# Performance work log

Hardware: AMD Instinct MI355X
Metric: run time of the kernel (lower is better)

Reference implementation:

```python
import jax, jax.numpy as jnp
import numpy as np

NUM_HEADS = 16
D_MODEL = 1024
BATCH = 4
SEQ = 1024


def setup_inputs() -> dict:
    key = jax.random.key(0)
    k_x, k_m, k_wqkv, k_bqkv, k_wo, k_bo = jax.random.split(key, 6)
    d = D_MODEL
    scale = 1.0 / np.sqrt(d)
    return {
        "x": jax.random.normal(k_x, (BATCH, SEQ, d), dtype=jnp.float32),
        "mask": jax.random.randint(k_m, (BATCH, SEQ, SEQ), 0, 2, dtype=jnp.int32),
        "Wqkv": jax.random.normal(k_wqkv, (d, 3 * d), dtype=jnp.float32) * scale,
        "bqkv": jax.random.normal(k_bqkv, (3 * d,), dtype=jnp.float32) * 0.02,
        "Wo": jax.random.normal(k_wo, (d, d), dtype=jnp.float32) * scale,
        "bo": jax.random.normal(k_bo, (d,), dtype=jnp.float32) * 0.02,
    }


def reference(x, mask, Wqkv, bqkv, Wo, bo):
    B, S, D = x.shape
    H = NUM_HEADS
    hd = D // H
    # fused QKV projection: [B,S,3D] -> [B,S,H,3*hd] -> [B,H,S,3*hd]
    qkv = (x @ Wqkv + bqkv).reshape(B, S, H, 3 * hd).transpose(0, 2, 1, 3)
    q, k, v = jnp.split(qkv, 3, axis=-1)  # each [B,H,S,hd]
    # scores [B,H,S,S], scaled by sqrt(head_dim)
    scores = jnp.einsum("bhqd,bhkd->bhqk", q, k) / jnp.sqrt(jnp.float32(hd))
    scores = jnp.where(mask[:, None, :, :] == 0, jnp.float32(-1e20), scores)
    attn = jax.nn.softmax(scores, axis=-1)
    vals = jnp.einsum("bhqk,bhkd->bhqd", attn, v)  # [B,H,S,hd]
    vals = vals.transpose(0, 2, 1, 3).reshape(B, S, D)
    return vals @ Wo + bo
```

## Files before the change

kernel.cpp:

```cpp
#include <hip/hip_runtime.h>
#include <cstddef>
#include <cstdint>

#define BATCH 4
#define SEQ   1024
#define DM    1024
#define NH    16
#define HD    64
#define D3    3072
#define LOG2E 1.44269504088896340736f
#define QSCALE (0.125f * LOG2E)

typedef _Float16 f16x8 __attribute__((ext_vector_type(8)));
typedef _Float16 f16x4 __attribute__((ext_vector_type(4)));
typedef __fp16   h16x2 __attribute__((ext_vector_type(2)));
typedef float    f32x4 __attribute__((ext_vector_type(4)));

#define MFMA16(a, b, c) __builtin_amdgcn_mfma_f32_16x16x32_f16((a), (b), (c), 0, 0, 0)
#define GLD_LDS16(gp, lp) \
  __builtin_amdgcn_global_load_lds((const __attribute__((address_space(1))) unsigned int*)(gp), \
                                   (__attribute__((address_space(3))) unsigned int*)(lp), 16, 0, 0)
#if __has_builtin(__builtin_amdgcn_exp2f)
#define EXP2(x) __builtin_amdgcn_exp2f(x)
#else
#define EXP2(x) exp2f(x)
#endif

__global__ __launch_bounds__(256) void cast_f16(const float* __restrict__ in,
                                                _Float16* __restrict__ out, int n8) {
  int i = blockIdx.x * 256 + threadIdx.x;
  if (i >= n8) return;
  float4 a = ((const float4*)in)[i * 2];
  float4 b = ((const float4*)in)[i * 2 + 1];
  f16x8 o;
  o[0] = (_Float16)a.x; o[1] = (_Float16)a.y; o[2] = (_Float16)a.z; o[3] = (_Float16)a.w;
  o[4] = (_Float16)b.x; o[5] = (_Float16)b.y; o[6] = (_Float16)b.z; o[7] = (_Float16)b.w;
  ((f16x8*)out)[i] = o;
}

__global__ __launch_bounds__(256) void transpose_cast(const float* __restrict__ W,
                                                      _Float16* __restrict__ WT,
                                                      int K, int N) {
  __shared__ _Float16 T[64 * 72];
  const int tid = threadIdx.x;
  const int r0 = blockIdx.y * 64, c0 = blockIdx.x * 64;
#pragma unroll
  for (int it = 0; it < 4; ++it) {
    const int row = it * 16 + (tid >> 4);
    const int col4 = (tid & 15) * 4;
    float4 wv = *(const float4*)(W + (size_t)(r0 + row) * N + c0 + col4);
    T[(col4 + 0) * 72 + row] = (_Float16)wv.x;
    T[(col4 + 1) * 72 + row] = (_Float16)wv.y;
    T[(col4 + 2) * 72 + row] = (_Float16)wv.z;
    T[(col4 + 3) * 72 + row] = (_Float16)wv.w;
  }
  __syncthreads();
#pragma unroll
  for (int it = 0; it < 2; ++it) {
    const int g = it * 256 + tid;
    const int col = g >> 3, seg = g & 7;
    *(f16x8*)(WT + (size_t)(c0 + col) * K + r0 + seg * 8) = *(const f16x8*)(T + col * 72 + seg * 8);
  }
}

__global__ __launch_bounds__(256) void pack_mask(const int* __restrict__ mask,
                                                 unsigned long long* __restrict__ mb) {
  const size_t i = (size_t)blockIdx.x * 256 + threadIdx.x;
  const int m = mask[i];
  unsigned long long bits = __ballot(m != 0);
  if ((threadIdx.x & 63) == 0) mb[i >> 6] = bits;
}

template <typename OutT, bool QKV, int TN>
__global__ __launch_bounds__(256) void gemm_bt(const _Float16* __restrict__ A,
                                               const _Float16* __restrict__ BT,
                                               const float* __restrict__ bias,
                                               OutT* __restrict__ C,
                                               _Float16* __restrict__ vTp,
                                               int M, int N, int K) {
  constexpr int NT = TN / 32;
  __shared__ _Float16 As[128 * 32];
  __shared__ _Float16 Bs[TN * 32];
  const int tid = threadIdx.x;
  const int l15 = tid & 15;
  const int quad = (tid & 63) >> 4;
  const int w = tid >> 6;
  const int wm = w >> 1, wn = w & 1;
  const int rowbase = blockIdx.y * 128;
  const int colbase = blockIdx.x * TN;

  f32x4 acc[4][NT];
#pragma unroll
  for (int mt = 0; mt < 4; ++mt)
#pragma unroll
    for (int nt = 0; nt < NT; ++nt) acc[mt][nt] = (f32x4){0.f, 0.f, 0.f, 0.f};

  const int g0 = tid, g1 = 256 + tid;
  const _Float16* Ag0 = A + (size_t)(rowbase + (g0 >> 2)) * K + (g0 & 3) * 8;
  const _Float16* Ag1 = A + (size_t)(rowbase + (g1 >> 2)) * K + (g1 & 3) * 8;
  const _Float16* Bg0 = BT + (size_t)(colbase + (g0 >> 2)) * K + (g0 & 3) * 8;
  const _Float16* Bg1 = BT + (size_t)(colbase + ((g1 >> 2) & (TN - 1))) * K + (g1 & 3) * 8;

  for (int k0 = 0; k0 < K; k0 += 32) {
    __syncthreads();
    GLD_LDS16(Ag0 + k0, As + g0 * 8);
    GLD_LDS16(Ag1 + k0, As + g1 * 8);
    GLD_LDS16(Bg0 + k0, Bs + g0 * 8);
    if constexpr (TN == 128) GLD_LDS16(Bg1 + k0, Bs + g1 * 8);
    __syncthreads();
    f16x8 a[4], b[NT];
#pragma unroll
    for (int mt = 0; mt < 4; ++mt)
      a[mt] = *(const f16x8*)(As + (wm * 64 + mt * 16 + l15) * 32 + quad * 8);
#pragma unroll
    for (int nt = 0; nt < NT; ++nt)
      b[nt] = *(const f16x8*)(Bs + (wn * (TN / 2) + nt * 16 + l15) * 32 + quad * 8);
#pragma unroll
    for (int mt = 0; mt < 4; ++mt)
#pragma unroll
      for (int nt = 0; nt < NT; ++nt)
        acc[mt][nt] = MFMA16(a[mt], b[nt], acc[mt][nt]);
  }

  float bv[NT];
#pragma unroll
  for (int nt = 0; nt < NT; ++nt) bv[nt] = bias[colbase + wn * (TN / 2) + nt * 16 + l15];
#pragma unroll
  for (int mt = 0; mt < 4; ++mt)
#pragma unroll
    for (int nt = 0; nt < NT; ++nt) {
      const int col = colbase + wn * (TN / 2) + nt * 16 + l15;
      if (QKV) {
        const int reg3 = (col >> 6) % 3;
        if (reg3 == 2) {
          const int hh = col / 192;
          const int d = col - hh * 192 - 128;
          const int row0 = rowbase + wm * 64 + mt * 16 + quad * 4;
          const int bb = row0 >> 10, s0 = row0 & 1023;
          f16x4 pk;
#pragma unroll
          for (int r = 0; r < 4; ++r) pk[r] = (_Float16)(acc[mt][nt][r] + bv[nt]);
          *(f16x4*)(vTp + ((size_t)((bb * NH + hh) * HD + d)) * SEQ + s0) = pk;
        } else {
          const float sc = (reg3 == 0) ? QSCALE : 1.f;
#pragma unroll
          for (int r = 0; r < 4; ++r) {
            const int row = rowbase + wm * 64 + mt * 16 + quad * 4 + r;
            C[(size_t)row * N + col] = (OutT)((acc[mt][nt][r] + bv[nt]) * sc);
          }
        }
      } else {
#pragma unroll
        for (int r = 0; r < 4; ++r) {
          const int row = rowbase + wm * 64 + mt * 16 + quad * 4 + r;
          C[(size_t)row * N + col] = (OutT)(acc[mt][nt][r] + bv[nt]);
        }
      }
    }
}

__global__ __launch_bounds__(256) void attn(const _Float16* __restrict__ qkv,
                                            const _Float16* __restrict__ vT,
                                            const unsigned long long* __restrict__ mb,
                                            _Float16* __restrict__ vals) {
  __shared__ _Float16 Ks[64 * 72];
  __shared__ _Float16 Vt[64 * 72];
  __shared__ _Float16 Ps[4][32 * 72];
  __shared__ __align__(8) _Float16 LUT[16][4];
  const int tid = threadIdx.x;
  const int l15 = tid & 15, quad = (tid & 63) >> 4, w = tid >> 6;
  const int b = blockIdx.y >> 4, h = blockIdx.y & 15;
  const int q0 = blockIdx.x << 7;

  if (tid < 16) {
    LUT[tid][0] = (tid & 1) ? (_Float16)1.f : (_Float16)0.f;
    LUT[tid][1] = (tid & 2) ? (_Float16)1.f : (_Float16)0.f;
    LUT[tid][2] = (tid & 4) ? (_Float16)1.f : (_Float16)0.f;
    LUT[tid][3] = (tid & 8) ? (_Float16)1.f : (_Float16)0.f;
  }

  const _Float16* qb = qkv + (size_t)b * SEQ * D3 + h * 192;
  f16x8 qf[2][2];
#pragma unroll
  for (int qn = 0; qn < 2; ++qn)
#pragma unroll
    for (int hf = 0; hf < 2; ++hf)
      qf[qn][hf] = *(const f16x8*)(qb + (size_t)(q0 + w * 32 + qn * 16 + l15) * D3 +
                                   hf * 32 + quad * 8);

  const _Float16* kg = qb + 64;
  const _Float16* vg = vT + (size_t)((b * NH + h) * HD) * SEQ;
  const int sr = tid >> 3, sseg = tid & 7;
  const int vd = tid >> 2, vs = tid & 3;
  const size_t mb0 = (size_t)(b * SEQ + q0 + w * 32 + l15) * 16;
  const size_t mb1 = (size_t)(b * SEQ + q0 + w * 32 + 16 + l15) * 16;

  f16x8 k0r = *(const f16x8*)(kg + (size_t)sr * D3 + sseg * 8);
  f16x8 k1r = *(const f16x8*)(kg + (size_t)(sr + 32) * D3 + sseg * 8);
  f16x8 v0r = *(const f16x8*)(vg + (size_t)vd * SEQ + vs * 8);
  f16x8 v1r = *(const f16x8*)(vg + (size_t)vd * SEQ + 32 + vs * 8);
  unsigned long long mr0 = mb[mb0], mr1 = mb[mb1];

  f32x4 lacc[2];
  f32x4 o_[2][4];
#pragma unroll
  for (int qn = 0; qn < 2; ++qn) {
    lacc[qn] = (f32x4){0.f, 0.f, 0.f, 0.f};
#pragma unroll
    for (int dt = 0; dt < 4; ++dt) o_[qn][dt] = (f32x4){0.f, 0.f, 0.f, 0.f};
  }
  f16x8 ones;
#pragma unroll
  for (int i = 0; i < 8; ++i) ones[i] = (_Float16)1.f;

  for (int kt = 0; kt < 16; ++kt) {
    if (kt) __syncthreads();
    *(f16x8*)(Ks + sr * 72 + sseg * 8) = k0r;
    *(f16x8*)(Ks + (sr + 32) * 72 + sseg * 8) = k1r;
    *(f16x8*)(Vt + vd * 72 + vs * 8) = v0r;
    *(f16x8*)(Vt + vd * 72 + 32 + vs * 8) = v1r;
    __syncthreads();
    const unsigned long long mc[2] = {mr0, mr1};
    if (kt < 15) {
      const int kn = (kt + 1) << 6;
      k0r = *(const f16x8*)(kg + (size_t)(kn + sr) * D3 + sseg * 8);
      k1r = *(const f16x8*)(kg + (size_t)(kn + sr + 32) * D3 + sseg * 8);
      v0r = *(const f16x8*)(vg + (size_t)vd * SEQ + kn + vs * 8);
      v1r = *(const f16x8*)(vg + (size_t)vd * SEQ + kn + 32 + vs * 8);
      mr0 = mb[mb0 + kt + 1];
      mr1 = mb[mb1 + kt + 1];
    }
    f32x4 st[4][2];
#pragma unroll
    for (int mt = 0; mt < 4; ++mt)
#pragma unroll
      for (int qn = 0; qn < 2; ++qn) st[mt][qn] = (f32x4){0.f, 0.f, 0.f, 0.f};
#pragma unroll
    for (int mt = 0; mt < 4; ++mt) {
      f16x8 ka0 = *(const f16x8*)(Ks + (mt * 16 + l15) * 72 + quad * 8);
      f16x8 ka1 = *(const f16x8*)(Ks + (mt * 16 + l15) * 72 + 32 + quad * 8);
#pragma unroll
      for (int qn = 0; qn < 2; ++qn) {
        st[mt][qn] = MFMA16(ka0, qf[qn][0], st[mt][qn]);
        st[mt][qn] = MFMA16(ka1, qf[qn][1], st[mt][qn]);
      }
    }
#pragma unroll
    for (int qn = 0; qn < 2; ++qn)
#pragma unroll
      for (int mt = 0; mt < 4; ++mt) {
        float e0 = EXP2(fminf(st[mt][qn][0], 15.f));
        float e1 = EXP2(fminf(st[mt][qn][1], 15.f));
        float e2 = EXP2(fminf(st[mt][qn][2], 15.f));
        float e3 = EXP2(fminf(st[mt][qn][3], 15.f));
        h16x2 lo = __builtin_amdgcn_cvt_pkrtz(e0, e1);
        h16x2 hi = __builtin_amdgcn_cvt_pkrtz(e2, e3);
        f16x4 pk;
        pk[0] = (_Float16)lo[0]; pk[1] = (_Float16)lo[1];
        pk[2] = (_Float16)hi[0]; pk[3] = (_Float16)hi[1];
        const unsigned nib = (unsigned)(mc[qn] >> (mt * 16 + quad * 4)) & 15u;
        pk *= *(const f16x4*)LUT[nib];
        *(f16x4*)(&Ps[w][(qn * 16 + l15) * 72 + mt * 16 + quad * 4]) = pk;
      }
    f16x8 pa[2][2];
#pragma unroll
    for (int qn = 0; qn < 2; ++qn) {
      pa[qn][0] = *(const f16x8*)(&Ps[w][(qn * 16 + l15) * 72 + quad * 8]);
      pa[qn][1] = *(const f16x8*)(&Ps[w][(qn * 16 + l15) * 72 + 32 + quad * 8]);
      lacc[qn] = MFMA16(pa[qn][0], ones, lacc[qn]);
      lacc[qn] = MFMA16(pa[qn][1], ones, lacc[qn]);
    }
#pragma unroll
    for (int dt = 0; dt < 4; ++dt) {
      f16x8 vb0 = *(const f16x8*)(Vt + (dt * 16 + l15) * 72 + quad * 8);
      f16x8 vb1 = *(const f16x8*)(Vt + (dt * 16 + l15) * 72 + 32 + quad * 8);
#pragma unroll
      for (int qn = 0; qn < 2; ++qn) {
        o_[qn][dt] = MFMA16(pa[qn][0], vb0, o_[qn][dt]);
        o_[qn][dt] = MFMA16(pa[qn][1], vb1, o_[qn][dt]);
      }
    }
  }
#pragma unroll
  for (int qn = 0; qn < 2; ++qn) {
    f32x4 inv;
#pragma unroll
    for (int r = 0; r < 4; ++r) inv[r] = 1.f / lacc[qn][r];
#pragma unroll
    for (int dt = 0; dt < 4; ++dt)
#pragma unroll
      for (int r = 0; r < 4; ++r)
        vals[(size_t)(b * SEQ + q0 + w * 32 + qn * 16 + quad * 4 + r) * DM +
             h * HD + dt * 16 + l15] = (_Float16)(o_[qn][dt][r] * inv[r]);
  }
}

extern "C" void kernel_launch(void* const* d_in, const int* in_sizes, int n_in,
                              void* d_out, int out_size, void* d_ws, size_t ws_size,
                              hipStream_t stream) {
  const float* x    = (const float*)d_in[0];
  const int*   mask = (const int*)  d_in[1];
  const float* Wqkv = (const float*)d_in[2];
  const float* bqkv = (const float*)d_in[3];
  const float* Wo   = (const float*)d_in[4];
  const float* bo   = (const float*)d_in[5];
  float* out = (float*)d_out;

  char* ws = (char*)d_ws;
  _Float16* qkv16  = (_Float16*)ws;                    ws += (size_t)BATCH*SEQ*D3*2;
  _Float16* vT16   = (_Float16*)ws;                    ws += (size_t)BATCH*DM*SEQ*2;
  _Float16* x16    = (_Float16*)ws;                    ws += (size_t)BATCH*SEQ*DM*2;
  _Float16* WqkvT  = (_Float16*)ws;                    ws += (size_t)DM*D3*2;
  _Float16* WoT    = (_Float16*)ws;                    ws += (size_t)DM*DM*2;
  _Float16* vals16 = (_Float16*)ws;                    ws += (size_t)BATCH*SEQ*DM*2;
  unsigned long long* mbits = (unsigned long long*)ws;

  cast_f16<<<(BATCH*SEQ*DM/8 + 255)/256, 256, 0, stream>>>(x, x16, BATCH*SEQ*DM/8);
  transpose_cast<<<dim3(D3/64, DM/64), 256, 0, stream>>>(Wqkv, WqkvT, DM, D3);
  transpose_cast<<<dim3(DM/64, DM/64), 256, 0, stream>>>(Wo, WoT, DM, DM);
  pack_mask<<<(BATCH*SEQ*SEQ)/256, 256, 0, stream>>>(mask, mbits);

  gemm_bt<_Float16, true, 128><<<dim3(D3/128, BATCH*SEQ/128), 256, 0, stream>>>(
      x16, WqkvT, bqkv, qkv16, vT16, BATCH*SEQ, D3, DM);
  attn<<<dim3(SEQ/128, BATCH*NH), 256, 0, stream>>>(qkv16, vT16, mbits, vals16);
  gemm_bt<float, false, 64><<<dim3(DM/64, (BATCH*SEQ)/128), 256, 0, stream>>>(
      vals16, WoT, bo, out, nullptr, BATCH*SEQ, DM, DM);
}
```

Baseline: 203.1 us.

## Merge prep kernels, deepen GEMM K-tile with swizzled LDS, remap attention grid

Fuses the x cast and mask packing into one launch, and the two weight transposes into another, cutting the number of kernel launches. The GEMM now stages 64-wide K tiles with an XOR-swizzled LDS layout, which halves barrier count and avoids bank conflicts, at the cost of more LDS per block. The attention grid becomes 1D with a block-index remap that groups heads, intended to improve L2 locality for the mask and K/V.

```diff
diff --git a/kernel.cpp b/kernel.cpp
--- a/kernel.cpp
+++ b/kernel.cpp
@@ -26,24 +26,40 @@
 #define EXP2(x) exp2f(x)
 #endif
 
-__global__ __launch_bounds__(256) void cast_f16(const float* __restrict__ in,
-                                                _Float16* __restrict__ out, int n8) {
-  int i = blockIdx.x * 256 + threadIdx.x;
-  if (i >= n8) return;
-  float4 a = ((const float4*)in)[i * 2];
-  float4 b = ((const float4*)in)[i * 2 + 1];
-  f16x8 o;
-  o[0] = (_Float16)a.x; o[1] = (_Float16)a.y; o[2] = (_Float16)a.z; o[3] = (_Float16)a.w;
-  o[4] = (_Float16)b.x; o[5] = (_Float16)b.y; o[6] = (_Float16)b.z; o[7] = (_Float16)b.w;
-  ((f16x8*)out)[i] = o;
-}
-
-__global__ __launch_bounds__(256) void transpose_cast(const float* __restrict__ W,
-                                                      _Float16* __restrict__ WT,
-                                                      int K, int N) {
+__global__ __launch_bounds__(256) void prep(const float* __restrict__ x,
+                                            _Float16* __restrict__ x16,
+                                            const int* __restrict__ mask,
+                                            unsigned long long* __restrict__ mb) {
+  const int tid = threadIdx.x;
+  if (blockIdx.x < 2048) {
+    const int i = blockIdx.x * 256 + tid;
+    float4 a = ((const float4*)x)[i * 2];
+    float4 b = ((const float4*)x)[i * 2 + 1];
+    f16x8 o;
+    o[0] = (_Float16)a.x; o[1] = (_Float16)a.y; o[2] = (_Float16)a.z; o[3] = (_Float16)a.w;
+    o[4] = (_Float16)b.x; o[5] = (_Float16)b.y; o[6] = (_Float16)b.z; o[7] = (_Float16)b.w;
+    ((f16x8*)x16)[i] = o;
+  } else {
+    const size_t i = (size_t)(blockIdx.x - 2048) * 256 + tid;
+    const int m = mask[i];
+    unsigned long long bits = __ballot(m != 0);
+    if ((tid & 63) == 0) mb[i >> 6] = bits;
+  }
+}
+
+__global__ __launch_bounds__(256) void transpose_cast2(const float* __restrict__ W1,
+                                                       _Float16* __restrict__ WT1,
+                                                       const float* __restrict__ W2,
+                                                       _Float16* __restrict__ WT2) {
   __shared__ _Float16 T[64 * 72];
   const int tid = threadIdx.x;
-  const int r0 = blockIdx.y * 64, c0 = blockIdx.x * 64;
+  const bool first = blockIdx.x < 48;
+  const float* W = first ? W1 : W2;
+  _Float16* WT = first ? WT1 : WT2;
+  const int N = first ? D3 : DM;
+  const int K = DM;
+  const int c0 = (first ? blockIdx.x : (blockIdx.x - 48)) * 64;
+  const int r0 = blockIdx.y * 64;
 #pragma unroll
   for (int it = 0; it < 4; ++it) {
     const int row = it * 16 + (tid >> 4);
@@ -63,14 +79,6 @@
   }
 }
 
-__global__ __launch_bounds__(256) void pack_mask(const int* __restrict__ mask,
-                                                 unsigned long long* __restrict__ mb) {
-  const size_t i = (size_t)blockIdx.x * 256 + threadIdx.x;
-  const int m = mask[i];
-  unsigned long long bits = __ballot(m != 0);
-  if ((threadIdx.x & 63) == 0) mb[i >> 6] = bits;
-}
-
 template <typename OutT, bool QKV, int TN>
 __global__ __launch_bounds__(256) void gemm_bt(const _Float16* __restrict__ A,
                                                const _Float16* __restrict__ BT,
@@ -79,8 +87,8 @@
                                                _Float16* __restrict__ vTp,
                                                int M, int N, int K) {
   constexpr int NT = TN / 32;
-  __shared__ _Float16 As[128 * 32];
-  __shared__ _Float16 Bs[TN * 32];
+  __shared__ _Float16 As[128 * 64];
+  __shared__ _Float16 Bs[TN * 64];
   const int tid = threadIdx.x;
   const int l15 = tid & 15;
   const int quad = (tid & 63) >> 4;
@@ -95,31 +103,40 @@
 #pragma unroll
     for (int nt = 0; nt < NT; ++nt) acc[mt][nt] = (f32x4){0.f, 0.f, 0.f, 0.f};
 
-  const int g0 = tid, g1 = 256 + tid;
-  const _Float16* Ag0 = A + (size_t)(rowbase + (g0 >> 2)) * K + (g0 & 3) * 8;
-  const _Float16* Ag1 = A + (size_t)(rowbase + (g1 >> 2)) * K + (g1 & 3) * 8;
-  const _Float16* Bg0 = BT + (size_t)(colbase + (g0 >> 2)) * K + (g0 & 3) * 8;
-  const _Float16* Bg1 = BT + (size_t)(colbase + ((g1 >> 2) & (TN - 1))) * K + (g1 & 3) * 8;
-
-  for (int k0 = 0; k0 < K; k0 += 32) {
+  for (int k0 = 0; k0 < K; k0 += 64) {
     __syncthreads();
-    GLD_LDS16(Ag0 + k0, As + g0 * 8);
-    GLD_LDS16(Ag1 + k0, As + g1 * 8);
-    GLD_LDS16(Bg0 + k0, Bs + g0 * 8);
-    if constexpr (TN == 128) GLD_LDS16(Bg1 + k0, Bs + g1 * 8);
+#pragma unroll
+    for (int it = 0; it < 4; ++it) {
+      const int g = it * 256 + tid;
+      const int r = g >> 3, cs = (g & 7) ^ (r & 7);
+      GLD_LDS16(A + (size_t)(rowbase + r) * K + k0 + cs * 8, As + g * 8);
+    }
+#pragma unroll
+    for (int it = 0; it < TN / 32; ++it) {
+      const int g = it * 256 + tid;
+      const int r = g >> 3, cs = (g & 7) ^ (r & 7);
+      GLD_LDS16(BT + (size_t)(colbase + r) * K + k0 + cs * 8, Bs + g * 8);
+    }
     __syncthreads();
-    f16x8 a[4], b[NT];
-#pragma unroll
-    for (int mt = 0; mt < 4; ++mt)
-      a[mt] = *(const f16x8*)(As + (wm * 64 + mt * 16 + l15) * 32 + quad * 8);
-#pragma unroll
-    for (int nt = 0; nt < NT; ++nt)
-      b[nt] = *(const f16x8*)(Bs + (wn * (TN / 2) + nt * 16 + l15) * 32 + quad * 8);
-#pragma unroll
-    for (int mt = 0; mt < 4; ++mt)
-#pragma unroll
-      for (int nt = 0; nt < NT; ++nt)
-        acc[mt][nt] = MFMA16(a[mt], b[nt], acc[mt][nt]);
+#pragma unroll
+    for (int kh = 0; kh < 2; ++kh) {
+      f16x8 a[4], b[NT];
+#pragma unroll
+      for (int mt = 0; mt < 4; ++mt) {
+        const int row = wm * 64 + mt * 16 + l15;
+        a[mt] = *(const f16x8*)(As + row * 64 + (((kh * 4 + quad) ^ (row & 7)) << 3));
+      }
+#pragma unroll
+      for (int nt = 0; nt < NT; ++nt) {
+        const int row = wn * (TN / 2) + nt * 16 + l15;
+        b[nt] = *(const f16x8*)(Bs + row * 64 + (((kh * 4 + quad) ^ (row & 7)) << 3));
+      }
+#pragma unroll
+      for (int mt = 0; mt < 4; ++mt)
+#pragma unroll
+        for (int nt = 0; nt < NT; ++nt)
+          acc[mt][nt] = MFMA16(a[mt], b[nt], acc[mt][nt]);
+    }
   }
 
   float bv[NT];
@@ -169,8 +186,10 @@
   __shared__ __align__(8) _Float16 LUT[16][4];
   const int tid = threadIdx.x;
   const int l15 = tid & 15, quad = (tid & 63) >> 4, w = tid >> 6;
-  const int b = blockIdx.y >> 4, h = blockIdx.y & 15;
-  const int q0 = blockIdx.x << 7;
+  const int i = blockIdx.x;
+  const int bh = (i >> 6) * 8 + (i & 7);
+  const int b = bh >> 4, h = bh & 15;
+  const int q0 = ((i >> 3) & 7) << 7;
 
   if (tid < 16) {
     LUT[tid][0] = (tid & 1) ? (_Float16)1.f : (_Float16)0.f;
@@ -211,7 +230,7 @@
   }
   f16x8 ones;
 #pragma unroll
-  for (int i = 0; i < 8; ++i) ones[i] = (_Float16)1.f;
+  for (int i2 = 0; i2 < 8; ++i2) ones[i2] = (_Float16)1.f;
 
   for (int kt = 0; kt < 16; ++kt) {
     if (kt) __syncthreads();
@@ -315,14 +334,12 @@
   _Float16* vals16 = (_Float16*)ws;                    ws += (size_t)BATCH*SEQ*DM*2;
   unsigned long long* mbits = (unsigned long long*)ws;
 
-  cast_f16<<<(BATCH*SEQ*DM/8 + 255)/256, 256, 0, stream>>>(x, x16, BATCH*SEQ*DM/8);
-  transpose_cast<<<dim3(D3/64, DM/64), 256, 0, stream>>>(Wqkv, WqkvT, DM, D3);
-  transpose_cast<<<dim3(DM/64, DM/64), 256, 0, stream>>>(Wo, WoT, DM, DM);
-  pack_mask<<<(BATCH*SEQ*SEQ)/256, 256, 0, stream>>>(mask, mbits);
+  prep<<<2048 + (BATCH*SEQ*SEQ)/256, 256, 0, stream>>>(x, x16, mask, mbits);
+  transpose_cast2<<<dim3(64, 16), 256, 0, stream>>>(Wqkv, WqkvT, Wo, WoT);
 
   gemm_bt<_Float16, true, 128><<<dim3(D3/128, BATCH*SEQ/128), 256, 0, stream>>>(
       x16, WqkvT, bqkv, qkv16, vT16, BATCH*SEQ, D3, DM);
-  attn<<<dim3(SEQ/128, BATCH*NH), 256, 0, stream>>>(qkv16, vT16, mbits, vals16);
+  attn<<<512, 256, 0, stream>>>(qkv16, vT16, mbits, vals16);
   gemm_bt<float, false, 64><<<dim3(DM/64, (BATCH*SEQ)/128), 256, 0, stream>>>(
       vals16, WoT, bo, out, nullptr, BATCH*SEQ, DM, DM);
 }
```

Result: faster. 185.8 us (-8.5%).
